# Kernel tuning notes

Measured on AMD Instinct MI355X. Metric: run time of the kernel, lower is better.

## Reference

```python
import jax, jax.numpy as jnp
import numpy as np

D = 1024
B, S = 4, 2048


def setup_inputs() -> dict:
    key = jax.random.key(0)
    ks = jax.random.split(key, 6)
    sc = 1.0 / np.sqrt(D)  # truncated-normal-ish fan-in scale like hk.Linear default
    return {
        "x": jax.random.normal(ks[0], (B, S, D), dtype=jnp.float32),
        "W_amp1": jax.random.normal(ks[1], (D, D), dtype=jnp.float32) * sc,
        "b_amp1": jnp.zeros((D,), dtype=jnp.float32),
        "W_amp2": jax.random.normal(ks[2], (D, D), dtype=jnp.float32) * sc,
        "b_amp2": jnp.zeros((D,), dtype=jnp.float32),
        "vqc_params": jax.random.uniform(ks[3], (D, 4), dtype=jnp.float32, minval=-np.pi, maxval=np.pi),
        "W_post1": jax.random.normal(ks[4], (D, D), dtype=jnp.float32) * sc,
        "b_post1": jnp.zeros((D,), dtype=jnp.float32),
        "W_post2": jax.random.normal(ks[5], (D, D), dtype=jnp.float32) * sc,
        "b_post2": jnp.zeros((D,), dtype=jnp.float32),
    }


def reference(x, W_amp1, b_amp1, W_amp2, b_amp2, vqc_params,
              W_post1, b_post1, W_post2, b_post2):
    # amplitude encoder: Linear -> tanh -> Linear
    amp = jnp.tanh(x @ W_amp1 + b_amp1) @ W_amp2 + b_amp2  # [B,S,D]

    # variational quantum circuit, vectorized over channels:
    # per-channel i: out_i = amp_i*cos(theta_i/2) + Re(amp_i*sin(theta_i/2)*e^{i phi_i})
    #              = amp_i * (cos(theta_i/2) + sin(theta_i/2)*cos(phi_i))
    theta = vqc_params[:, 0]  # [D]
    phi = vqc_params[:, 1]    # [D]
    scale = jnp.cos(theta * 0.5) + jnp.sin(theta * 0.5) * jnp.cos(phi)  # [D]
    q = amp * scale  # broadcast over [B,S,D]

    # classical post: Linear -> silu -> Linear
    out = jax.nn.silu(q @ W_post1 + b_post1) @ W_post2 + b_post2
    return out
```

## Files before the change

kernel.cpp:

```cpp
#include <hip/hip_runtime.h>
#include <hip/hip_bf16.h>
#include <math.h>

#define DD 1024
#define MM 8192

typedef __attribute__((ext_vector_type(8))) short short8;
typedef __attribute__((ext_vector_type(4))) float f32x4;

__device__ inline unsigned short f32_to_bf16(float f) {
  union { float f; unsigned u; } v; v.f = f;
  unsigned u = v.u;
  u += 0x7FFFu + ((u >> 16) & 1u);
  return (unsigned short)(u >> 16);
}

__global__ void k_prep(const float* __restrict__ x, unsigned short* __restrict__ xb,
                       const float* __restrict__ w0, const float* __restrict__ w1,
                       const float* __restrict__ w2, const float* __restrict__ w3,
                       unsigned short* __restrict__ o0, unsigned short* __restrict__ o1,
                       unsigned short* __restrict__ o2, unsigned short* __restrict__ o3,
                       const float* __restrict__ vqc, float* __restrict__ sc) {
  const int bid = blockIdx.x, tid = threadIdx.x;
  if (bid < 4096) {
    const float4* xv = (const float4*)x;
    ushort4* ov = (ushort4*)xb;
    int i = bid * 256 + tid;
    #pragma unroll
    for (int r = 0; r < 2; r++, i += 4096 * 256) {
      float4 v = xv[i];
      ushort4 u;
      u.x = f32_to_bf16(v.x); u.y = f32_to_bf16(v.y);
      u.z = f32_to_bf16(v.z); u.w = f32_to_bf16(v.w);
      ov[i] = u;
    }
  } else if (bid < 8192) {
    const int rel = bid - 4096;
    const float* src; unsigned short* dst;
    switch (rel >> 10) {
      case 0: src = w0; dst = o0; break;
      case 1: src = w1; dst = o1; break;
      case 2: src = w2; dst = o2; break;
      default: src = w3; dst = o3; break;
    }
    const int t = rel & 1023;
    const int r0 = (t >> 5) * 32, c0 = (t & 31) * 32;
    __shared__ float tl[32][33];
    const int tx = tid & 31, ty = tid >> 5;
    #pragma unroll
    for (int i = 0; i < 4; i++)
      tl[ty + 8 * i][tx] = src[(size_t)(r0 + ty + 8 * i) * DD + c0 + tx];
    __syncthreads();
    #pragma unroll
    for (int i = 0; i < 4; i++)
      dst[(size_t)(c0 + ty + 8 * i) * DD + r0 + tx] = f32_to_bf16(tl[tx][ty + 8 * i]);
  } else {
    #pragma unroll
    for (int k = 0; k < 4; k++) {
      int d = tid + k * 256;
      float th = vqc[d * 4 + 0] * 0.5f, ph = vqc[d * 4 + 1];
      sc[d] = cosf(th) + sinf(th) * cosf(ph);
    }
  }
}

template <int EPI>
__launch_bounds__(256, 3)
__global__ void k_gemm(const unsigned short* __restrict__ A,
                       const unsigned short* __restrict__ Bt,
                       const float* __restrict__ bias,
                       const float* __restrict__ scale,
                       void* __restrict__ Cout) {
  constexpr int K = DD, N = DD;
  constexpr int NT = K / 64;
  __shared__ unsigned short As[2][128 * 64];
  __shared__ unsigned short Bs[2][64 * 64];
  const int tid = threadIdx.x;
  const int wave = tid >> 6, lane = tid & 63;
  const int wr = wave >> 1, wc = wave & 1;

  const int L = blockIdx.y * gridDim.x + blockIdx.x;
  const int bx = (L >> 3) & 15;
  const int by = (L & 7) | ((L >> 7) << 3);
  const int rowA0 = by * 128, colB0 = bx * 64;

  const int lr = lane & 15, lk = (lane >> 4) * 8;
  const int srow = lane >> 3;
  const int sswz = ((lane & 7) ^ srow) * 8;

  const unsigned short* gA[4];
  const unsigned short* gB[2];
  #pragma unroll
  for (int i = 0; i < 4; i++)
    gA[i] = A + (size_t)(rowA0 + i * 32 + wave * 8 + srow) * K + sswz;
  #pragma unroll
  for (int j = 0; j < 2; j++)
    gB[j] = Bt + (size_t)(colB0 + j * 32 + wave * 8 + srow) * K + sswz;

  auto STAGE = [&](int buf, int t) {
    const int ko = t * 64;
    #pragma unroll
    for (int i = 0; i < 4; i++)
      __builtin_amdgcn_global_load_lds(
          (const __attribute__((address_space(1))) unsigned int*)(gA[i] + ko),
          (__attribute__((address_space(3))) unsigned int*)(&As[buf][(i * 32 + wave * 8) * 64]),
          16, 0, 0);
    #pragma unroll
    for (int j = 0; j < 2; j++)
      __builtin_amdgcn_global_load_lds(
          (const __attribute__((address_space(1))) unsigned int*)(gB[j] + ko),
          (__attribute__((address_space(3))) unsigned int*)(&Bs[buf][(j * 32 + wave * 8) * 64]),
          16, 0, 0);
  };

  f32x4 acc[4][2] = {};

  STAGE(0, 0);
  for (int t = 0; t < NT; ++t) {
    const int cur = t & 1;
    if (t + 1 < NT) {
      STAGE(cur ^ 1, t + 1);
      asm volatile("s_waitcnt vmcnt(6)\ns_barrier" ::: "memory");
    } else {
      asm volatile("s_waitcnt vmcnt(0)\ns_barrier" ::: "memory");
    }

    #pragma unroll
    for (int kk = 0; kk < 64; kk += 32) {
      short8 a[4], b[2];
      #pragma unroll
      for (int m = 0; m < 4; m++) {
        int row = wr * 64 + m * 16 + lr;
        a[m] = *(const short8*)(&As[cur][row * 64 + ((((kk + lk) >> 3) ^ (row & 7)) << 3)]);
      }
      #pragma unroll
      for (int n = 0; n < 2; n++) {
        int row = wc * 32 + n * 16 + lr;
        b[n] = *(const short8*)(&Bs[cur][row * 64 + ((((kk + lk) >> 3) ^ (row & 7)) << 3)]);
      }
      #pragma unroll
      for (int m = 0; m < 4; m++)
        #pragma unroll
        for (int n = 0; n < 2; n++)
          acc[m][n] = __builtin_amdgcn_mfma_f32_16x16x32_bf16(a[m], b[n], acc[m][n], 0, 0, 0);
    }
    __builtin_amdgcn_s_barrier();
  }

  const int row0 = rowA0 + wr * 64;
  const int col0 = colB0 + wc * 32;
  #pragma unroll
  for (int n = 0; n < 2; n++) {
    const int col = col0 + n * 16 + lr;
    const float bv = bias[col];
    const float sv = (EPI == 1) ? scale[col] : 0.f;
    #pragma unroll
    for (int m = 0; m < 4; m++) {
      #pragma unroll
      for (int j = 0; j < 4; j++) {
        int row = row0 + m * 16 + (lane >> 4) * 4 + j;
        float z = acc[m][n][j] + bv;
        if constexpr (EPI == 0) {
          ((unsigned short*)Cout)[(size_t)row * N + col] = f32_to_bf16(tanhf(z));
        } else if constexpr (EPI == 1) {
          ((unsigned short*)Cout)[(size_t)row * N + col] = f32_to_bf16(z * sv);
        } else if constexpr (EPI == 2) {
          ((unsigned short*)Cout)[(size_t)row * N + col] = f32_to_bf16(z / (1.f + __expf(-z)));
        } else {
          ((float*)Cout)[(size_t)row * N + col] = z;
        }
      }
    }
  }
}

extern "C" void kernel_launch(void* const* d_in, const int* in_sizes, int n_in,
                              void* d_out, int out_size, void* d_ws, size_t ws_size,
                              hipStream_t stream) {
  const float* x   = (const float*)d_in[0];
  const float* W1  = (const float*)d_in[1];
  const float* b1  = (const float*)d_in[2];
  const float* W2  = (const float*)d_in[3];
  const float* b2  = (const float*)d_in[4];
  const float* vqc = (const float*)d_in[5];
  const float* Wp1 = (const float*)d_in[6];
  const float* bp1 = (const float*)d_in[7];
  const float* Wp2 = (const float*)d_in[8];
  const float* bp2 = (const float*)d_in[9];

  char* ws = (char*)d_ws;
  unsigned short* actA = (unsigned short*)ws;
  unsigned short* actB = (unsigned short*)(ws + (16u << 20));
  unsigned short* Wt0  = (unsigned short*)(ws + (32u << 20));
  unsigned short* Wt1  = (unsigned short*)(ws + (34u << 20));
  unsigned short* Wt2  = (unsigned short*)(ws + (36u << 20));
  unsigned short* Wt3  = (unsigned short*)(ws + (38u << 20));
  float* scale = (float*)(ws + (40u << 20));

  k_prep<<<8193, 256, 0, stream>>>(x, actA, W1, W2, Wp1, Wp2,
                                   Wt0, Wt1, Wt2, Wt3, vqc, scale);

  dim3 g(DD / 64, MM / 128), b(256);
  k_gemm<0><<<g, b, 0, stream>>>(actA, Wt0, b1,  nullptr, actB);
  k_gemm<1><<<g, b, 0, stream>>>(actB, Wt1, b2,  scale,   actA);
  k_gemm<2><<<g, b, 0, stream>>>(actA, Wt2, bp1, nullptr, actB);
  k_gemm<3><<<g, b, 0, stream>>>(actB, Wt3, bp2, nullptr, d_out);
}
```

Measured before the change: 134.3 us.

## Enlarge GEMM tiles to 256x128 with 8 waves and triple-buffered interleaved loads

```diff
diff --git a/kernel.cpp b/kernel.cpp
--- a/kernel.cpp
+++ b/kernel.cpp
@@ -65,7 +65,7 @@
 }
 
 template <int EPI>
-__launch_bounds__(256, 3)
+__launch_bounds__(512, 2)
 __global__ void k_gemm(const unsigned short* __restrict__ A,
                        const unsigned short* __restrict__ Bt,
                        const float* __restrict__ bias,
@@ -73,18 +73,19 @@
                        void* __restrict__ Cout) {
   constexpr int K = DD, N = DD;
   constexpr int NT = K / 64;
-  __shared__ unsigned short As[2][128 * 64];
-  __shared__ unsigned short Bs[2][64 * 64];
+  __shared__ unsigned short As[3][256 * 64];
+  __shared__ unsigned short Bs[3][128 * 64];
   const int tid = threadIdx.x;
   const int wave = tid >> 6, lane = tid & 63;
-  const int wr = wave >> 1, wc = wave & 1;
+  const int wr = wave >> 2, wc = wave & 3;
 
   const int L = blockIdx.y * gridDim.x + blockIdx.x;
-  const int bx = (L >> 3) & 15;
-  const int by = (L & 7) | ((L >> 7) << 3);
-  const int rowA0 = by * 128, colB0 = bx * 64;
-
-  const int lr = lane & 15, lk = (lane >> 4) * 8;
+  const int bx = (L >> 3) & 7;
+  const int by = (L & 7) | ((L >> 6) << 3);
+  const int rowA0 = by * 256, colB0 = bx * 128;
+
+  const int lr = lane & 15;
+  const int lks = lane >> 4;
   const int srow = lane >> 3;
   const int sswz = ((lane & 7) ^ srow) * 8;
 
@@ -92,62 +93,85 @@
   const unsigned short* gB[2];
   #pragma unroll
   for (int i = 0; i < 4; i++)
-    gA[i] = A + (size_t)(rowA0 + i * 32 + wave * 8 + srow) * K + sswz;
+    gA[i] = A + (size_t)(rowA0 + i * 64 + wave * 8 + srow) * K + sswz;
   #pragma unroll
   for (int j = 0; j < 2; j++)
-    gB[j] = Bt + (size_t)(colB0 + j * 32 + wave * 8 + srow) * K + sswz;
-
-  auto STAGE = [&](int buf, int t) {
-    const int ko = t * 64;
-    #pragma unroll
-    for (int i = 0; i < 4; i++)
-      __builtin_amdgcn_global_load_lds(
-          (const __attribute__((address_space(1))) unsigned int*)(gA[i] + ko),
-          (__attribute__((address_space(3))) unsigned int*)(&As[buf][(i * 32 + wave * 8) * 64]),
-          16, 0, 0);
-    #pragma unroll
-    for (int j = 0; j < 2; j++)
-      __builtin_amdgcn_global_load_lds(
-          (const __attribute__((address_space(1))) unsigned int*)(gB[j] + ko),
-          (__attribute__((address_space(3))) unsigned int*)(&Bs[buf][(j * 32 + wave * 8) * 64]),
-          16, 0, 0);
+    gB[j] = Bt + (size_t)(colB0 + j * 64 + wave * 8 + srow) * K + sswz;
+
+  auto stageA = [&](int buf, int t, int i) {
+    __builtin_amdgcn_global_load_lds(
+        (const __attribute__((address_space(1))) unsigned int*)(gA[i] + t * 64),
+        (__attribute__((address_space(3))) unsigned int*)(&As[buf][(i * 64 + wave * 8) * 64]),
+        16, 0, 0);
   };
-
-  f32x4 acc[4][2] = {};
-
-  STAGE(0, 0);
+  auto stageB = [&](int buf, int t, int j) {
+    __builtin_amdgcn_global_load_lds(
+        (const __attribute__((address_space(1))) unsigned int*)(gB[j] + t * 64),
+        (__attribute__((address_space(3))) unsigned int*)(&Bs[buf][(j * 64 + wave * 8) * 64]),
+        16, 0, 0);
+  };
+
+  f32x4 acc[8][2] = {};
+
+  #pragma unroll
+  for (int i = 0; i < 4; i++) stageA(0, 0, i);
+  #pragma unroll
+  for (int j = 0; j < 2; j++) stageB(0, 0, j);
+  #pragma unroll
+  for (int i = 0; i < 4; i++) stageA(1, 1, i);
+  #pragma unroll
+  for (int j = 0; j < 2; j++) stageB(1, 1, j);
+  asm volatile("s_waitcnt vmcnt(6)\ns_barrier" ::: "memory");
+
   for (int t = 0; t < NT; ++t) {
-    const int cur = t & 1;
-    if (t + 1 < NT) {
-      STAGE(cur ^ 1, t + 1);
-      asm volatile("s_waitcnt vmcnt(6)\ns_barrier" ::: "memory");
-    } else {
-      asm volatile("s_waitcnt vmcnt(0)\ns_barrier" ::: "memory");
-    }
-
-    #pragma unroll
-    for (int kk = 0; kk < 64; kk += 32) {
+    const int cur = t % 3;
+    const bool st = (t + 2 < NT);
+    const int sbuf = (t + 2) % 3;
+
+    #pragma unroll
+    for (int ph = 0; ph < 4; ++ph) {
+      const int h = ph >> 1, kk = ph & 1;
+
       short8 a[4], b[2];
       #pragma unroll
-      for (int m = 0; m < 4; m++) {
-        int row = wr * 64 + m * 16 + lr;
-        a[m] = *(const short8*)(&As[cur][row * 64 + ((((kk + lk) >> 3) ^ (row & 7)) << 3)]);
+      for (int m2 = 0; m2 < 4; m2++) {
+        int row = wr * 128 + h * 64 + m2 * 16 + lr;
+        a[m2] = *(const short8*)(&As[cur][row * 64 + (((kk * 4 + lks) ^ (row & 7)) << 3)]);
       }
       #pragma unroll
       for (int n = 0; n < 2; n++) {
         int row = wc * 32 + n * 16 + lr;
-        b[n] = *(const short8*)(&Bs[cur][row * 64 + ((((kk + lk) >> 3) ^ (row & 7)) << 3)]);
-      }
-      #pragma unroll
-      for (int m = 0; m < 4; m++)
+        b[n] = *(const short8*)(&Bs[cur][row * 64 + (((kk * 4 + lks) ^ (row & 7)) << 3)]);
+      }
+
+      if (st) {
+        if (ph == 0) { stageA(sbuf, t + 2, 0); stageA(sbuf, t + 2, 1); }
+        else if (ph == 1) { stageA(sbuf, t + 2, 2); stageA(sbuf, t + 2, 3); }
+        else if (ph == 2) { stageB(sbuf, t + 2, 0); }
+        else { stageB(sbuf, t + 2, 1); }
+      }
+
+      asm volatile("s_barrier" ::: "memory");
+      __builtin_amdgcn_s_setprio(1);
+      #pragma unroll
+      for (int m2 = 0; m2 < 4; m2++)
         #pragma unroll
         for (int n = 0; n < 2; n++)
-          acc[m][n] = __builtin_amdgcn_mfma_f32_16x16x32_bf16(a[m], b[n], acc[m][n], 0, 0, 0);
-    }
-    __builtin_amdgcn_s_barrier();
+          acc[h * 4 + m2][n] =
+              __builtin_amdgcn_mfma_f32_16x16x32_bf16(a[m2], b[n], acc[h * 4 + m2][n], 0, 0, 0);
+      __builtin_amdgcn_s_setprio(0);
+      __builtin_amdgcn_sched_barrier(0);
+
+      if (ph < 3) {
+        asm volatile("s_barrier" ::: "memory");
+      } else if (t + 1 < NT) {
+        if (st) asm volatile("s_waitcnt vmcnt(6)\ns_barrier" ::: "memory");
+        else    asm volatile("s_waitcnt vmcnt(0)\ns_barrier" ::: "memory");
+      }
+    }
   }
 
-  const int row0 = rowA0 + wr * 64;
+  const int row0 = rowA0 + wr * 128;
   const int col0 = colB0 + wc * 32;
   #pragma unroll
   for (int n = 0; n < 2; n++) {
@@ -155,11 +179,11 @@
     const float bv = bias[col];
     const float sv = (EPI == 1) ? scale[col] : 0.f;
     #pragma unroll
-    for (int m = 0; m < 4; m++) {
+    for (int f = 0; f < 8; f++) {
       #pragma unroll
       for (int j = 0; j < 4; j++) {
-        int row = row0 + m * 16 + (lane >> 4) * 4 + j;
-        float z = acc[m][n][j] + bv;
+        int row = row0 + f * 16 + lks * 4 + j;
+        float z = acc[f][n][j] + bv;
         if constexpr (EPI == 0) {
           ((unsigned short*)Cout)[(size_t)row * N + col] = f32_to_bf16(tanhf(z));
         } else if constexpr (EPI == 1) {
@@ -200,7 +224,7 @@
   k_prep<<<8193, 256, 0, stream>>>(x, actA, W1, W2, Wp1, Wp2,
                                    Wt0, Wt1, Wt2, Wt3, vqc, scale);
 
-  dim3 g(DD / 64, MM / 128), b(256);
+  dim3 g(DD / 128, MM / 256), b(512);
   k_gemm<0><<<g, b, 0, stream>>>(actA, Wt0, b1,  nullptr, actB);
   k_gemm<1><<<g, b, 0, stream>>>(actB, Wt1, b2,  scale,   actA);
   k_gemm<2><<<g, b, 0, stream>>>(actA, Wt2, bp1, nullptr, actB);
```

Result: slower. 140.9 us (+5.0%).
